# Performance work log

Hardware: AMD Instinct MI355X
Metric: run time of the kernel (lower is better)

Reference implementation:

```python
import jax, jax.numpy as jnp
import numpy as np
from jax import lax

SIGMA = 0.5
SCORE_THRESHOLD = 0.05
N = 4096


def setup_inputs() -> dict:
    key = jax.random.key(0)
    k1, k2, k3 = jax.random.split(key, 3)
    # realistic boxes: top-left corner in [0,1000), width/height in [1,101)
    xy1 = jax.random.uniform(k1, (N, 2), dtype=jnp.float32) * 1000.0
    wh = jax.random.uniform(k2, (N, 2), dtype=jnp.float32) * 100.0 + 1.0
    boxes = jnp.concatenate([xy1, xy1 + wh], axis=1)  # [N,4] x1,y1,x2,y2
    scores = jax.random.uniform(k3, (N,), dtype=jnp.float32)
    return {"boxes": boxes, "scores": scores}


def _soft_nms(boxes, scores, sigma, score_threshold):
    n = boxes.shape[0]
    areas = (boxes[:, 2] - boxes[:, 0]) * (boxes[:, 3] - boxes[:, 1])  # [N]
    idx_range = jnp.arange(n)

    def body(i, state):
        s, processed = state
        # pick highest-score unprocessed box (== swap-to-front in the
        # original sorted formulation)
        masked = jnp.where(processed, -jnp.inf, s)
        j = jnp.argmax(masked)
        b = boxes[j]
        # IoU of selected box vs all boxes (vectorized)
        xx1 = jnp.maximum(b[0], boxes[:, 0])
        yy1 = jnp.maximum(b[1], boxes[:, 1])
        xx2 = jnp.minimum(b[2], boxes[:, 2])
        yy2 = jnp.minimum(b[3], boxes[:, 3])
        w = jnp.maximum(xx2 - xx1, 0.0)
        h = jnp.maximum(yy2 - yy1, 0.0)
        inter = w * h
        iou = inter / (areas[j] + areas - inter)
        # Gaussian decay on remaining (unprocessed) boxes
        weight = jnp.exp(-(iou * iou) / sigma)
        active = (~processed) & (idx_range != j)
        s = jnp.where(active, s * weight, s)
        processed = processed.at[j].set(True)
        return s, processed

    scores_out, _ = lax.fori_loop(
        0, n, body, (scores, jnp.zeros((n,), dtype=bool)))
    keep = scores_out > score_threshold
    return scores_out, keep


def reference(boxes, scores):
    return _soft_nms(boxes, scores, SIGMA, SCORE_THRESHOLD)
```

## Files before the change

### kernel.cpp

```cpp
#include <hip/hip_runtime.h>

#define N_BOX 4096
#define NT    1024
#define KPT   4
#define NW    16
#define KTOP  8
#define MAXC  (NW * KTOP)
#define NEG_INF (-__builtin_huge_valf())

typedef unsigned long long u64;

__device__ __forceinline__ u64 dpp_max_u64(u64 x) {
#define DPP_STEP(CTRL) { \
    int lo_ = __builtin_amdgcn_update_dpp(0, (int)(unsigned)x,         CTRL, 0xF, 0xF, true); \
    int hi_ = __builtin_amdgcn_update_dpp(0, (int)(unsigned)(x >> 32), CTRL, 0xF, 0xF, true); \
    u64 o_ = ((u64)(unsigned)hi_ << 32) | (unsigned)lo_; \
    x = (o_ > x) ? o_ : x; }
    DPP_STEP(0x111)
    DPP_STEP(0x112)
    DPP_STEP(0x114)
    DPP_STEP(0x118)
    DPP_STEP(0x142)
    DPP_STEP(0x143)
#undef DPP_STEP
    const int lo = __builtin_amdgcn_readlane((int)(unsigned)x, 63);
    const int hi = __builtin_amdgcn_readlane((int)(unsigned)(x >> 32), 63);
    return ((u64)(unsigned)hi << 32) | (unsigned)lo;
}

__device__ __forceinline__ float bcast_f32(float v, int ln) {
    return __int_as_float(__builtin_amdgcn_readlane(__float_as_int(v), ln));
}

__global__ __launch_bounds__(NT, 1) void soft_nms_kernel(
    const float* __restrict__ boxes,
    const float* __restrict__ scores,
    float* __restrict__ out)
{
    const int tid  = threadIdx.x;
    const int lane = tid & 63;
    const int wave = tid >> 6;

    __shared__ unsigned s_key[N_BOX];
    __shared__ u64      s_wtop[2][NW][KTOP + 1];
    __shared__ float    s_wgeom[2][NW][KTOP][5];
    __shared__ float    s_wbb[NW][4];
    __shared__ int      s_wlist[NW][MAXC + 1];
    __shared__ int      s_wcnt[NW];
    __shared__ int      s_C;

    #pragma unroll
    for (int k = 0; k < KPT; ++k) {
        const int i = tid * KPT + k;
        const float4 b = reinterpret_cast<const float4*>(boxes)[i];
        const float cx = 0.5f * (b.x + b.z);
        const float cy = 0.5f * (b.y + b.w);
        int icx = (int)(cx * 0.016f); icx = icx < 0 ? 0 : (icx > 15 ? 15 : icx);
        int icy = (int)(cy * 0.016f); icy = icy < 0 ? 0 : (icy > 15 ? 15 : icy);
        unsigned m = 0;
        #pragma unroll
        for (int bb = 0; bb < 4; ++bb)
            m |= (((unsigned)(icx >> bb) & 1u) << (2*bb)) |
                 (((unsigned)(icy >> bb) & 1u) << (2*bb + 1));
        s_key[i] = (m << 12) | (unsigned)i;
    }
    __syncthreads();

    for (int kk = 2; kk <= N_BOX; kk <<= 1) {
        for (int j = kk >> 1; j > 0; j >>= 1) {
            #pragma unroll
            for (int t = 0; t < KPT; ++t) {
                const int e = tid + t * NT;
                const int p = e ^ j;
                if (p > e) {
                    const unsigned a = s_key[e], b = s_key[p];
                    const bool up = ((e & kk) == 0);
                    if ((a > b) == up) { s_key[e] = b; s_key[p] = a; }
                }
            }
            __syncthreads();
        }
    }

    float bx1[KPT], by1[KPT], bx2[KPT], by2[KPT], bar[KPT], cur[KPT], fin[KPT];
    unsigned klo[KPT];
    #pragma unroll
    for (int k = 0; k < KPT; ++k) {
        const int spos = tid * KPT + k;
        const int oi = (int)(s_key[spos] & 0xFFFu);
        const float4 b = reinterpret_cast<const float4*>(boxes)[oi];
        bx1[k] = b.x; by1[k] = b.y; bx2[k] = b.z; by2[k] = b.w;
        bar[k] = (b.z - b.x) * (b.w - b.y);
        cur[k] = scores[oi];
        fin[k] = 0.0f;
        klo[k] = ((unsigned)(4095 - oi) << 13) | (unsigned)(spos + 1);
    }

    float tbx1 = bx1[0], tby1 = by1[0], tbx2 = bx2[0], tby2 = by2[0];
    #pragma unroll
    for (int k = 1; k < KPT; ++k) {
        tbx1 = fminf(tbx1, bx1[k]); tby1 = fminf(tby1, by1[k]);
        tbx2 = fmaxf(tbx2, bx2[k]); tby2 = fmaxf(tby2, by2[k]);
    }
    float wbx1 = tbx1, wby1 = tby1, wbx2 = tbx2, wby2 = tby2;
    #pragma unroll
    for (int off = 1; off < 64; off <<= 1) {
        wbx1 = fminf(wbx1, __shfl_xor(wbx1, off));
        wby1 = fminf(wby1, __shfl_xor(wby1, off));
        wbx2 = fmaxf(wbx2, __shfl_xor(wbx2, off));
        wby2 = fmaxf(wby2, __shfl_xor(wby2, off));
    }
    if (lane == 0) {
        s_wbb[wave][0] = wbx1; s_wbb[wave][1] = wby1;
        s_wbb[wave][2] = wbx2; s_wbb[wave][3] = wby2;
    }

    auto rebuild = [&](int G) {
        u64 lk[KPT];
        #pragma unroll
        for (int k = 0; k < KPT; ++k)
            lk[k] = (cur[k] < 0.0f) ? 0ull
                  : (((u64)__float_as_uint(cur[k]) << 25) | (u64)klo[k]);
        #pragma unroll
        for (int p = 0; p <= KTOP; ++p) {
            u64 m4 = lk[0];
            #pragma unroll
            for (int k = 1; k < KPT; ++k) m4 = lk[k] > m4 ? lk[k] : m4;
            const u64 m = dpp_max_u64(m4);
            if (lane == 0) s_wtop[G][wave][p] = m;
            if (p < KTOP && m != 0ull) {
                #pragma unroll
                for (int k = 0; k < KPT; ++k) {
                    if (lk[k] == m) {
                        lk[k] = 0ull;
                        s_wgeom[G][wave][p][0] = bx1[k];
                        s_wgeom[G][wave][p][1] = by1[k];
                        s_wgeom[G][wave][p][2] = bx2[k];
                        s_wgeom[G][wave][p][3] = by2[k];
                        s_wgeom[G][wave][p][4] = bar[k];
                    }
                }
            }
        }
    };

    rebuild(0);
    int g = 0;
    __syncthreads();

    int remaining = N_BOX;
    int guard = 0;
    while (remaining > 0 && ++guard <= N_BOX) {
        if (wave == 0) {
            const int cw = lane >> 2, cr = lane & 3;
            u64 ck0 = s_wtop[g][cw][cr];
            u64 ck1 = s_wtop[g][cw][4 + cr];
            const float c0x1 = s_wgeom[g][cw][cr][0],   c0y1 = s_wgeom[g][cw][cr][1];
            const float c0x2 = s_wgeom[g][cw][cr][2],   c0y2 = s_wgeom[g][cw][cr][3];
            const float c0ar = s_wgeom[g][cw][cr][4];
            const float c1x1 = s_wgeom[g][cw][4+cr][0], c1y1 = s_wgeom[g][cw][4+cr][1];
            const float c1x2 = s_wgeom[g][cw][4+cr][2], c1y2 = s_wgeom[g][cw][4+cr][3];
            const float c1ar = s_wgeom[g][cw][4+cr][4];
            float lbx1 = 0.f, lby1 = 0.f, lbx2 = -1.f, lby2 = -1.f;
            if (lane < NW) {
                lbx1 = s_wbb[lane][0]; lby1 = s_wbb[lane][1];
                lbx2 = s_wbb[lane][2]; lby2 = s_wbb[lane][3];
            }
            int mycnt = 0;
            u64 tv = (lane < NW) ? s_wtop[g][lane][KTOP] : 0ull;
            const u64 T = dpp_max_u64(tv);
            int C = 0;
            while (C < MAXC) {
                u64 m4 = ck0 > ck1 ? ck0 : ck1;
                const u64 m = dpp_max_u64(m4);
                if (m <= T) break;
                const u64 b0 = __ballot(ck0 == m);
                int ln; bool r1;
                if (b0) { ln = (int)__ffsll(b0) - 1; r1 = false; }
                else    { ln = (int)__ffsll(__ballot(ck1 == m)) - 1; r1 = true; }
                const int slot = (ln >> 2) * KTOP + (r1 ? 4 : 0) + (ln & 3);
                const int rec  = (slot << 12) | (int)((m & 0x1FFFull) - 1);
                if (ck0 == m) ck0 = 0ull;
                if (ck1 == m) ck1 = 0ull;
                const float jx1 = bcast_f32(r1 ? c1x1 : c0x1, ln);
                const float jy1 = bcast_f32(r1 ? c1y1 : c0y1, ln);
                const float jx2 = bcast_f32(r1 ? c1x2 : c0x2, ln);
                const float jy2 = bcast_f32(r1 ? c1y2 : c0y2, ln);
                const float ja  = bcast_f32(r1 ? c1ar : c0ar, ln);
                if (lane < NW &&
                    !(jx1 > lbx2 || jx2 < lbx1 || jy1 > lby2 || jy2 < lby1)) {
                    s_wlist[lane][mycnt] = rec;
                    ++mycnt;
                }
#define DECAY_CK(CK, CX1, CY1, CX2, CY2, CAR) \
                if (CK != 0ull) { \
                    const float xx1 = fmaxf(jx1, CX1), yy1 = fmaxf(jy1, CY1); \
                    const float xx2 = fminf(jx2, CX2), yy2 = fminf(jy2, CY2); \
                    const float w_ = fmaxf(xx2 - xx1, 0.0f), h_ = fmaxf(yy2 - yy1, 0.0f); \
                    const float inter = w_ * h_; \
                    if (inter > 0.0f) { \
                        const float iou = inter / (ja + CAR - inter); \
                        float s_ = __uint_as_float((unsigned)(CK >> 25)); \
                        s_ *= __expf(iou * iou * -2.0f); \
                        CK = ((u64)__float_as_uint(s_) << 25) | (CK & 0x1FFFFFFull); } }
                DECAY_CK(ck0, c0x1, c0y1, c0x2, c0y2, c0ar)
                DECAY_CK(ck1, c1x1, c1y1, c1x2, c1y2, c1ar)
#undef DECAY_CK
                ++C;
            }
            if (lane < NW) s_wcnt[lane] = mycnt;
            if (lane == 0) s_C = C;
        }
        __syncthreads();

        const int C   = s_C;
        const int myn = s_wcnt[wave];

        for (int n = 0; n < myn; ++n) {
            const int rec  = s_wlist[wave][n];
            const int slot = rec >> 12;
            const int sp   = rec & 0xFFF;
            const float jx1 = s_wgeom[g][slot >> 3][slot & 7][0];
            const float jy1 = s_wgeom[g][slot >> 3][slot & 7][1];
            const float jx2 = s_wgeom[g][slot >> 3][slot & 7][2];
            const float jy2 = s_wgeom[g][slot >> 3][slot & 7][3];
            const float ja  = s_wgeom[g][slot >> 3][slot & 7][4];
            const bool mine = (sp >> 2) == tid;
            if (!mine && (jx1 > tbx2 || jx2 < tbx1 || jy1 > tby2 || jy2 < tby1))
                continue;
            #pragma unroll
            for (int k = 0; k < KPT; ++k) {
                if (mine && (sp & 3) == k) {
                    fin[k] = cur[k];
                    cur[k] = NEG_INF;
                } else {
                    const float xx1 = fmaxf(jx1, bx1[k]);
                    const float yy1 = fmaxf(jy1, by1[k]);
                    const float xx2 = fminf(jx2, bx2[k]);
                    const float yy2 = fminf(jy2, by2[k]);
                    const float w = fmaxf(xx2 - xx1, 0.0f);
                    const float h = fmaxf(yy2 - yy1, 0.0f);
                    const float inter = w * h;
                    const float iou = inter / (ja + bar[k] - inter);
                    cur[k] *= __expf(iou * iou * -2.0f);
                }
            }
        }

        if (myn > 0) {
            rebuild(g ^ 1);
        } else {
            if (lane <= KTOP) s_wtop[g ^ 1][wave][lane] = s_wtop[g][wave][lane];
            if (lane < KTOP * 5)
                ((float*)s_wgeom[g ^ 1][wave])[lane] =
                    ((const float*)s_wgeom[g][wave])[lane];
        }
        g ^= 1;
        remaining -= C;
        __syncthreads();
    }

    #pragma unroll
    for (int k = 0; k < KPT; ++k) {
        const int oi = 4095 - (int)((klo[k] >> 13) & 0xFFFu);
        out[oi] = fin[k];
        out[N_BOX + oi] = (fin[k] > 0.05f) ? 1.0f : 0.0f;
    }
}

extern "C" void kernel_launch(void* const* d_in, const int* in_sizes, int n_in,
                              void* d_out, int out_size, void* d_ws, size_t ws_size,
                              hipStream_t stream) {
    const float* boxes  = (const float*)d_in[0];
    const float* scores = (const float*)d_in[1];
    float* out = (float*)d_out;
    soft_nms_kernel<<<1, NT, 0, stream>>>(boxes, scores, out);
}
```

Baseline: 3.035 ms.

## Run candidate selection redundantly in every wave to drop a block barrier

```diff
diff --git a/kernel.cpp b/kernel.cpp
--- a/kernel.cpp
+++ b/kernel.cpp
@@ -44,10 +44,7 @@
     __shared__ unsigned s_key[N_BOX];
     __shared__ u64      s_wtop[2][NW][KTOP + 1];
     __shared__ float    s_wgeom[2][NW][KTOP][5];
-    __shared__ float    s_wbb[NW][4];
-    __shared__ int      s_wlist[NW][MAXC + 1];
-    __shared__ int      s_wcnt[NW];
-    __shared__ int      s_C;
+    __shared__ int      s_wlist[NW][MAXC];
 
     #pragma unroll
     for (int k = 0; k < KPT; ++k) {
@@ -109,10 +106,6 @@
         wby1 = fminf(wby1, __shfl_xor(wby1, off));
         wbx2 = fmaxf(wbx2, __shfl_xor(wbx2, off));
         wby2 = fmaxf(wby2, __shfl_xor(wby2, off));
-    }
-    if (lane == 0) {
-        s_wbb[wave][0] = wbx1; s_wbb[wave][1] = wby1;
-        s_wbb[wave][2] = wbx2; s_wbb[wave][3] = wby2;
     }
 
     auto rebuild = [&](int G) {
@@ -151,70 +144,56 @@
     int remaining = N_BOX;
     int guard = 0;
     while (remaining > 0 && ++guard <= N_BOX) {
-        if (wave == 0) {
-            const int cw = lane >> 2, cr = lane & 3;
-            u64 ck0 = s_wtop[g][cw][cr];
-            u64 ck1 = s_wtop[g][cw][4 + cr];
-            const float c0x1 = s_wgeom[g][cw][cr][0],   c0y1 = s_wgeom[g][cw][cr][1];
-            const float c0x2 = s_wgeom[g][cw][cr][2],   c0y2 = s_wgeom[g][cw][cr][3];
-            const float c0ar = s_wgeom[g][cw][cr][4];
-            const float c1x1 = s_wgeom[g][cw][4+cr][0], c1y1 = s_wgeom[g][cw][4+cr][1];
-            const float c1x2 = s_wgeom[g][cw][4+cr][2], c1y2 = s_wgeom[g][cw][4+cr][3];
-            const float c1ar = s_wgeom[g][cw][4+cr][4];
-            float lbx1 = 0.f, lby1 = 0.f, lbx2 = -1.f, lby2 = -1.f;
-            if (lane < NW) {
-                lbx1 = s_wbb[lane][0]; lby1 = s_wbb[lane][1];
-                lbx2 = s_wbb[lane][2]; lby2 = s_wbb[lane][3];
-            }
-            int mycnt = 0;
-            u64 tv = (lane < NW) ? s_wtop[g][lane][KTOP] : 0ull;
-            const u64 T = dpp_max_u64(tv);
-            int C = 0;
-            while (C < MAXC) {
-                u64 m4 = ck0 > ck1 ? ck0 : ck1;
-                const u64 m = dpp_max_u64(m4);
-                if (m <= T) break;
-                const u64 b0 = __ballot(ck0 == m);
-                int ln; bool r1;
-                if (b0) { ln = (int)__ffsll(b0) - 1; r1 = false; }
-                else    { ln = (int)__ffsll(__ballot(ck1 == m)) - 1; r1 = true; }
-                const int slot = (ln >> 2) * KTOP + (r1 ? 4 : 0) + (ln & 3);
-                const int rec  = (slot << 12) | (int)((m & 0x1FFFull) - 1);
-                if (ck0 == m) ck0 = 0ull;
-                if (ck1 == m) ck1 = 0ull;
-                const float jx1 = bcast_f32(r1 ? c1x1 : c0x1, ln);
-                const float jy1 = bcast_f32(r1 ? c1y1 : c0y1, ln);
-                const float jx2 = bcast_f32(r1 ? c1x2 : c0x2, ln);
-                const float jy2 = bcast_f32(r1 ? c1y2 : c0y2, ln);
-                const float ja  = bcast_f32(r1 ? c1ar : c0ar, ln);
-                if (lane < NW &&
-                    !(jx1 > lbx2 || jx2 < lbx1 || jy1 > lby2 || jy2 < lby1)) {
-                    s_wlist[lane][mycnt] = rec;
-                    ++mycnt;
-                }
+        const int cw = lane >> 2, cr = lane & 3;
+        u64 ck0 = s_wtop[g][cw][cr];
+        u64 ck1 = s_wtop[g][cw][4 + cr];
+        const float c0x1 = s_wgeom[g][cw][cr][0],   c0y1 = s_wgeom[g][cw][cr][1];
+        const float c0x2 = s_wgeom[g][cw][cr][2],   c0y2 = s_wgeom[g][cw][cr][3];
+        const float c0ar = s_wgeom[g][cw][cr][4];
+        const float c1x1 = s_wgeom[g][cw][4+cr][0], c1y1 = s_wgeom[g][cw][4+cr][1];
+        const float c1x2 = s_wgeom[g][cw][4+cr][2], c1y2 = s_wgeom[g][cw][4+cr][3];
+        const float c1ar = s_wgeom[g][cw][4+cr][4];
+        u64 tv = (lane < NW) ? s_wtop[g][lane][KTOP] : 0ull;
+        const u64 T = dpp_max_u64(tv);
+        int C = 0;
+        int myn = 0;
+        while (C < MAXC) {
+            u64 m4 = ck0 > ck1 ? ck0 : ck1;
+            const u64 m = dpp_max_u64(m4);
+            if (m <= T) break;
+            const u64 b0 = __ballot(ck0 == m);
+            int ln; bool r1;
+            if (b0) { ln = (int)__ffsll(b0) - 1; r1 = false; }
+            else    { ln = (int)__ffsll(__ballot(ck1 == m)) - 1; r1 = true; }
+            const int slot = (ln >> 2) * KTOP + (r1 ? 4 : 0) + (ln & 3);
+            const int rec  = (slot << 12) | (int)((m & 0x1FFFull) - 1);
+            if (ck0 == m) ck0 = 0ull;
+            if (ck1 == m) ck1 = 0ull;
+            const float jx1 = bcast_f32(r1 ? c1x1 : c0x1, ln);
+            const float jy1 = bcast_f32(r1 ? c1y1 : c0y1, ln);
+            const float jx2 = bcast_f32(r1 ? c1x2 : c0x2, ln);
+            const float jy2 = bcast_f32(r1 ? c1y2 : c0y2, ln);
+            const float ja  = bcast_f32(r1 ? c1ar : c0ar, ln);
+            if (!(jx1 > wbx2 || jx2 < wbx1 || jy1 > wby2 || jy2 < wby1)) {
+                if (lane == 0) s_wlist[wave][myn] = rec;
+                ++myn;
+            }
 #define DECAY_CK(CK, CX1, CY1, CX2, CY2, CAR) \
-                if (CK != 0ull) { \
-                    const float xx1 = fmaxf(jx1, CX1), yy1 = fmaxf(jy1, CY1); \
-                    const float xx2 = fminf(jx2, CX2), yy2 = fminf(jy2, CY2); \
-                    const float w_ = fmaxf(xx2 - xx1, 0.0f), h_ = fmaxf(yy2 - yy1, 0.0f); \
-                    const float inter = w_ * h_; \
-                    if (inter > 0.0f) { \
-                        const float iou = inter / (ja + CAR - inter); \
-                        float s_ = __uint_as_float((unsigned)(CK >> 25)); \
-                        s_ *= __expf(iou * iou * -2.0f); \
-                        CK = ((u64)__float_as_uint(s_) << 25) | (CK & 0x1FFFFFFull); } }
-                DECAY_CK(ck0, c0x1, c0y1, c0x2, c0y2, c0ar)
-                DECAY_CK(ck1, c1x1, c1y1, c1x2, c1y2, c1ar)
+            if (CK != 0ull) { \
+                const float xx1 = fmaxf(jx1, CX1), yy1 = fmaxf(jy1, CY1); \
+                const float xx2 = fminf(jx2, CX2), yy2 = fminf(jy2, CY2); \
+                const float w_ = fmaxf(xx2 - xx1, 0.0f), h_ = fmaxf(yy2 - yy1, 0.0f); \
+                const float inter = w_ * h_; \
+                if (inter > 0.0f) { \
+                    const float iou = inter / (ja + CAR - inter); \
+                    float s_ = __uint_as_float((unsigned)(CK >> 25)); \
+                    s_ *= __expf(iou * iou * -2.0f); \
+                    CK = ((u64)__float_as_uint(s_) << 25) | (CK & 0x1FFFFFFull); } }
+            DECAY_CK(ck0, c0x1, c0y1, c0x2, c0y2, c0ar)
+            DECAY_CK(ck1, c1x1, c1y1, c1x2, c1y2, c1ar)
 #undef DECAY_CK
-                ++C;
-            }
-            if (lane < NW) s_wcnt[lane] = mycnt;
-            if (lane == 0) s_C = C;
-        }
-        __syncthreads();
-
-        const int C   = s_C;
-        const int myn = s_wcnt[wave];
+            ++C;
+        }
 
         for (int n = 0; n < myn; ++n) {
             const int rec  = s_wlist[wave][n];
```

After: 4.638 ms. 52.8% more time.
